# Performance work log

Measured on AMD Instinct MI355X. Metric: run time of the kernel, lower is better.

Reference implementation:

```python
import jax, jax.numpy as jnp
import numpy as np

DIM = 768
B, N = 8, 2048


def setup_inputs() -> dict:
    key = jax.random.key(0)
    k = jax.random.split(key, 8)
    s = 1.0 / np.sqrt(DIM)
    return {
        "x": jax.random.normal(k[0], (B, N, DIM), jnp.float32),
        "x2": jax.random.normal(k[1], (B, N, DIM), jnp.float32),
        "x3": jax.random.normal(k[2], (B, N, DIM), jnp.float32),
        "W1": jax.random.uniform(k[3], (DIM, DIM), jnp.float32, -s, s),
        "b1": jax.random.uniform(k[4], (DIM,), jnp.float32, -s, s),
        "W2": jax.random.uniform(k[5], (DIM, DIM), jnp.float32, -s, s),
        "b2": jax.random.uniform(k[6], (DIM,), jnp.float32, -s, s),
        "w": jnp.ones((1,), jnp.float32),
    }


def _cross_attention(x, x2, W, b):
    # key = softmax(x2.transpose(1,2), dim=1) -> softmax over feature axis, then [B, D, N]
    key = jnp.swapaxes(jax.nn.softmax(x2, axis=-1), 1, 2)  # [B, D, N]
    query = jax.nn.softmax(x2, axis=1)                      # [B, N, D], softmax over tokens
    context = jnp.einsum('bnd,bdm->bnm', x, key)            # [B, N, N]
    atten = jnp.einsum('bnm,bmd->bnd', context, query)      # [B, N, D]
    return atten @ W.T + b


def reference(x, x2, x3, W1, b1, W2, b2, w):
    a1 = _cross_attention(x, x2, W1, b1)
    a2 = _cross_attention(x, x3, W2, b2)
    f = jax.nn.sigmoid(w)  # scalar gate, broadcast
    atten = a1 * f + a2 * f
    return atten + x
```

## Files before the change

### kernel.cpp

```cpp
#include <hip/hip_runtime.h>

#define DIMD 768
#define NTOK 2048
#define NB   8

typedef __attribute__((ext_vector_type(8))) short bfrag8;
typedef __attribute__((ext_vector_type(4))) float accf4;

__device__ __forceinline__ unsigned short f2bf(float f) {
  unsigned u = __float_as_uint(f);
  return (unsigned short)((u + 0x7fffu + ((u >> 16) & 1u)) >> 16);
}

__device__ __forceinline__ void glds16(const void* g, void* l) {
  __builtin_amdgcn_global_load_lds(
      (const __attribute__((address_space(1))) void*)g,
      (__attribute__((address_space(3))) void*)l, 16, 0, 0);
}


__device__ __forceinline__ void packw_body(int blk, const float* __restrict__ W1,
                                           const float* __restrict__ W2,
                                           unsigned short* __restrict__ Wcat) {
  int gid = blk * 256 + threadIdx.x;
  int r = gid / 192, c4 = (gid % 192) * 4;
  float4 a = *(const float4*)(W1 + (size_t)r * DIMD + c4);
  float4 b = *(const float4*)(W2 + (size_t)r * DIMD + c4);
  union { unsigned short us[4]; uint2 u2; } ra, rb;
  ra.us[0] = f2bf(a.x); ra.us[1] = f2bf(a.y); ra.us[2] = f2bf(a.z); ra.us[3] = f2bf(a.w);
  rb.us[0] = f2bf(b.x); rb.us[1] = f2bf(b.y); rb.us[2] = f2bf(b.z); rb.us[3] = f2bf(b.w);
  *(uint2*)(Wcat + (size_t)r * 1536 + c4) = ra.u2;
  *(uint2*)(Wcat + (size_t)r * 1536 + 768 + c4) = rb.u2;
}

__device__ __forceinline__ void packx_body(int blk, const float* __restrict__ x,
                                           unsigned short* __restrict__ xb) {
  size_t gid = (size_t)blk * 256 + threadIdx.x;
  const float4* x4 = (const float4*)x;
  float4 v0 = x4[gid * 2], v1 = x4[gid * 2 + 1];
  union { unsigned short us[8]; uint4 u4; } r;
  r.us[0] = f2bf(v0.x); r.us[1] = f2bf(v0.y); r.us[2] = f2bf(v0.z); r.us[3] = f2bf(v0.w);
  r.us[4] = f2bf(v1.x); r.us[5] = f2bf(v1.y); r.us[6] = f2bf(v1.z); r.us[7] = f2bf(v1.w);
  ((uint4*)xb)[gid] = r.u4;
}

template <int TMD, int TND, int EPI>
__device__ __forceinline__ void gemm_body(
    unsigned short* As, unsigned short* Bs, int bid,
    const unsigned short* __restrict__ A, const unsigned short* __restrict__ B,
    void* __restrict__ Cout, int K, int lda, int ldb, int ldc, int ntx,
    long long sA, long long sB, long long sC,
    const float* __restrict__ wg, const float* __restrict__ b1v,
    const float* __restrict__ b2v, const float* __restrict__ xres) {
  constexpr int TM = 64 * TMD, TN = 64 * TND;
  constexpr int ASZ = TM * 64, BSZ = TN * 64;
  __shared__ float csi[64 * TND];
  const int t = threadIdx.x, w = t >> 6, lane = t & 63;
  const int bz = bid & 7;
  const int r = bid >> 3;
  const int by = r / ntx, bx = r - by * ntx;
  const int m0 = by * TM, n0 = bx * TN;
  const unsigned short* Ab = A + (size_t)bz * sA;
  const unsigned short* Bb = B + (size_t)bz * sB;
  const int srow = lane >> 3;
  const int scol = (lane & 7) * 8;

  auto stage = [&](int buf, int k0) {
    unsigned short* Ad = As + buf * ASZ;
    unsigned short* Bd = Bs + buf * BSZ;
#pragma unroll
    for (int l = 0; l < 2 * TND; ++l) {
      int chunk = l * 4 + w;
      int row = chunk * 8 + srow;
      glds16(Bb + (size_t)(n0 + row) * ldb + k0 + scol,
             (char*)Bd + chunk * 1024 + lane * 16);
    }
#pragma unroll
    for (int l = 0; l < 2 * TMD; ++l) {
      int chunk = l * 4 + w;
      int row = chunk * 8 + srow;
      glds16(Ab + (size_t)(m0 + row) * lda + k0 + scol,
             (char*)Ad + chunk * 1024 + lane * 16);
    }
  };

  stage(0, 0);

  if (EPI == 2) {
    for (int c = t; c < TN; c += 256) {
      const float* cp = b1v + (size_t)bz * 32 * DIMD + n0 + c;
      float s = 0.f;
#pragma unroll
      for (int p = 0; p < 32; ++p) s += cp[(size_t)p * DIMD];
      csi[c] = 1.0f / s;
    }
  }

  accf4 zero = {0.f, 0.f, 0.f, 0.f};
  accf4 acc[2 * TMD][2 * TND];
#pragma unroll
  for (int i = 0; i < 2 * TMD; ++i)
#pragma unroll
    for (int j = 0; j < 2 * TND; ++j) acc[i][j] = zero;

  const int wm = (w & 1) * (32 * TMD), wn = (w >> 1) * (32 * TND);
  const int lm = lane & 15, qd = lane >> 4;

  __syncthreads();

  const int nt = K / 64;
  int cur = 0;
#pragma unroll 2
  for (int tt = 0; tt < nt; ++tt) {
    if (tt + 1 < nt) stage(cur ^ 1, (tt + 1) * 64);
    const unsigned short* Ar = As + cur * ASZ;
    const unsigned short* Br = Bs + cur * BSZ;
#pragma unroll
    for (int kc = 0; kc < 2; ++kc) {
      bfrag8 av[2 * TMD], bv[2 * TND];
#pragma unroll
      for (int i = 0; i < 2 * TMD; ++i)
        av[i] = *(const bfrag8*)(Ar + (wm + i * 16 + lm) * 64 + kc * 32 + qd * 8);
#pragma unroll
      for (int j = 0; j < 2 * TND; ++j)
        bv[j] = *(const bfrag8*)(Br + (wn + j * 16 + lm) * 64 + kc * 32 + qd * 8);
      __builtin_amdgcn_s_setprio(1);
#pragma unroll
      for (int i = 0; i < 2 * TMD; ++i)
#pragma unroll
        for (int j = 0; j < 2 * TND; ++j)
          acc[i][j] = __builtin_amdgcn_mfma_f32_16x16x32_bf16(av[i], bv[j], acc[i][j], 0, 0, 0);
      __builtin_amdgcn_s_setprio(0);
    }
    if (tt + 1 < nt) {
      asm volatile("s_waitcnt vmcnt(0)\n\ts_barrier" ::: "memory");
    }
    cur ^= 1;
  }

  if (EPI == 0) {
    unsigned short* Cb = (unsigned short*)Cout + (size_t)bz * sC;
#pragma unroll
    for (int i = 0; i < 2 * TMD; ++i)
#pragma unroll
      for (int j = 0; j < 2 * TND; ++j) {
        int col = n0 + wn + j * 16 + lm;
#pragma unroll
        for (int rr = 0; rr < 4; ++rr) {
          int row = m0 + wm + i * 16 + qd * 4 + rr;
          Cb[(size_t)row * ldc + col] = f2bf(acc[i][j][rr]);
        }
      }
  } else if (EPI == 1) {
    float gate = 1.f / (1.f + __expf(-wg[0]));
    float* Co = (float*)Cout + (size_t)bz * sC;
    const float* Xr = xres + (size_t)bz * sC;
#pragma unroll
    for (int j = 0; j < 2 * TND; ++j) {
      int col = n0 + wn + j * 16 + lm;
      float gb = gate * (b1v[col] + b2v[col]);
#pragma unroll
      for (int i = 0; i < 2 * TMD; ++i)
#pragma unroll
        for (int rr = 0; rr < 4; ++rr) {
          int row = m0 + wm + i * 16 + qd * 4 + rr;
          size_t idx = (size_t)row * ldc + col;
          Co[idx] = gate * acc[i][j][rr] + gb + Xr[idx];
        }
    }
  } else {
    unsigned short* Cb = (unsigned short*)Cout + (size_t)bz * sC;
#pragma unroll
    for (int j = 0; j < 2 * TND; ++j) {
      int lc = wn + j * 16 + lm;
      int col = n0 + lc;
      float ci = csi[lc];
#pragma unroll
      for (int i = 0; i < 2 * TMD; ++i)
#pragma unroll
        for (int rr = 0; rr < 4; ++rr) {
          int row = m0 + wm + i * 16 + qd * 4 + rr;
          Cb[(size_t)row * ldc + col] = f2bf(acc[i][j][rr] * ci);
        }
    }
  }
}


__global__ __launch_bounds__(256) void prep_kernel(const float* __restrict__ W1,
                                                   const float* __restrict__ W2,
                                                   unsigned short* __restrict__ Wcat,
                                                   const float* __restrict__ x2,
                                                   const float* __restrict__ x3,
                                                   float* __restrict__ rs1,
                                                   float* __restrict__ rs2) {
  int blk = blockIdx.x;
  if (blk < 576) { packw_body(blk, W1, W2, Wcat); return; }
  int rblk = blk - 576;
  const float* src = (rblk < 4096) ? x2 : x3;
  float* dst = (rblk < 4096) ? rs1 : rs2;
  int q = rblk & 4095;
  int w = threadIdx.x >> 6, lane = threadIdx.x & 63;
  int row = q * 4 + w;
  const float* r = src + (size_t)row * DIMD;
  float s = 0.f;
#pragma unroll
  for (int j = 0; j < 12; ++j) s += __expf(r[lane + j * 64]);
#pragma unroll
  for (int off = 32; off; off >>= 1) s += __shfl_xor(s, off, 64);
  if (lane == 0) dst[row] = 1.0f / s;
}

__global__ __launch_bounds__(256) void sm_kq(
    const float* __restrict__ xA, const float* __restrict__ rsA,
    unsigned short* __restrict__ KtA, unsigned short* __restrict__ QtA,
    float* __restrict__ cspA,
    const float* __restrict__ xB, const float* __restrict__ rsB,
    unsigned short* __restrict__ KtB, unsigned short* __restrict__ QtB,
    float* __restrict__ cspB) {
  int z = blockIdx.z;
  const float* xin; const float* rsv; unsigned short* Kt; unsigned short* Qt;
  float* csp; int b;
  if (z < 8) { xin = xA; rsv = rsA; Kt = KtA; Qt = QtA; csp = cspA; b = z; }
  else       { xin = xB; rsv = rsB; Kt = KtB; Qt = QtB; csp = cspB; b = z - 8; }
  const int n0 = blockIdx.x * 64, dc = blockIdx.y;
  const int t = threadIdx.x;
  __shared__ float rowsi[64];
  __shared__ __align__(16) unsigned short etile[128 * 72];
  if (t < 64) rowsi[t] = rsv[(size_t)b * NTOK + n0 + t];
  const float* xbase = xin + ((size_t)b * NTOK + n0) * DIMD + dc * 128;
  const int tok = t >> 2, g0 = t & 3;
#pragma unroll
  for (int p = 0; p < 8; ++p) {
    int dg = g0 + p * 4;
    float4 v = *(const float4*)(xbase + (size_t)tok * DIMD + dg * 4);
    int dl = dg * 4;
    etile[(dl + 0) * 72 + tok] = f2bf(__expf(v.x));
    etile[(dl + 1) * 72 + tok] = f2bf(__expf(v.y));
    etile[(dl + 2) * 72 + tok] = f2bf(__expf(v.z));
    etile[(dl + 3) * 72 + tok] = f2bf(__expf(v.w));
  }
  __syncthreads();
#pragma unroll
  for (int q = 0; q < 4; ++q) {
    int dl = (t >> 3) + q * 32;
    int g = t & 7;
    uint4 e8 = *(const uint4*)(etile + dl * 72 + g * 8);
    float ef[8];
    ef[0] = __uint_as_float(e8.x << 16); ef[1] = __uint_as_float(e8.x & 0xffff0000u);
    ef[2] = __uint_as_float(e8.y << 16); ef[3] = __uint_as_float(e8.y & 0xffff0000u);
    ef[4] = __uint_as_float(e8.z << 16); ef[5] = __uint_as_float(e8.z & 0xffff0000u);
    ef[6] = __uint_as_float(e8.w << 16); ef[7] = __uint_as_float(e8.w & 0xffff0000u);
    float4 r0 = *(const float4*)&rowsi[g * 8];
    float4 r1 = *(const float4*)&rowsi[g * 8 + 4];
    union { unsigned short us[8]; uint4 u4; } ko;
    ko.us[0] = f2bf(ef[0] * r0.x); ko.us[1] = f2bf(ef[1] * r0.y);
    ko.us[2] = f2bf(ef[2] * r0.z); ko.us[3] = f2bf(ef[3] * r0.w);
    ko.us[4] = f2bf(ef[4] * r1.x); ko.us[5] = f2bf(ef[5] * r1.y);
    ko.us[6] = f2bf(ef[6] * r1.z); ko.us[7] = f2bf(ef[7] * r1.w);
    size_t orow = ((size_t)b * DIMD + dc * 128 + dl) * NTOK + n0 + g * 8;
    *(uint4*)(Kt + orow) = ko.u4;
    *(uint4*)(Qt + orow) = e8;
    float s = ((ef[0] + ef[1]) + (ef[2] + ef[3])) + ((ef[4] + ef[5]) + (ef[6] + ef[7]));
    s += __shfl_xor(s, 1, 64);
    s += __shfl_xor(s, 2, 64);
    s += __shfl_xor(s, 4, 64);
    if (g == 0) csp[((size_t)b * 32 + blockIdx.x) * DIMD + dc * 128 + dl] = s;
  }
}

template <int TMD, int TND, int EPI>
__global__ __launch_bounds__(256) void mfma_bt(
    const unsigned short* __restrict__ A, const unsigned short* __restrict__ B,
    void* __restrict__ Cout, int K, int lda, int ldb, int ldc, int ntx,
    long long sA, long long sB, long long sC,
    const float* __restrict__ wg, const float* __restrict__ b1v,
    const float* __restrict__ b2v, const float* __restrict__ xres) {
  __shared__ __align__(16) unsigned short As[2 * 64 * TMD * 64];
  __shared__ __align__(16) unsigned short Bs[2 * 64 * TND * 64];
  gemm_body<TMD, TND, EPI>(As, Bs, blockIdx.x, A, B, Cout, K, lda, ldb, ldc, ntx,
                           sA, sB, sC, wg, b1v, b2v, xres);
}

__global__ __launch_bounds__(256) void sgemm_s(
    const unsigned short* __restrict__ KtA, const unsigned short* __restrict__ QtA,
    const float* __restrict__ cspA,
    const unsigned short* __restrict__ KtB, const unsigned short* __restrict__ QtB,
    const float* __restrict__ cspB,
    unsigned short* __restrict__ Ca, unsigned short* __restrict__ Cb) {
  __shared__ __align__(16) unsigned short As[2 * 128 * 64];
  __shared__ __align__(16) unsigned short Bs[2 * 128 * 64];
  bool second = blockIdx.x >= 288;
  const unsigned short* A = second ? KtB : KtA;
  const unsigned short* B = second ? QtB : QtA;
  const float* csp = second ? cspB : cspA;
  unsigned short* C = second ? Cb : Ca;
  int blk = second ? (blockIdx.x - 288) : blockIdx.x;
  gemm_body<2, 2, 2>(As, Bs, blk, A, B, C, NTOK, NTOK, NTOK, 1536, 6,
                     768LL * NTOK, 768LL * NTOK, 768LL * 1536,
                     nullptr, csp, nullptr, nullptr);
}

__global__ __launch_bounds__(256) void s2_packx_kernel(
    const unsigned short* __restrict__ Wcat, const unsigned short* __restrict__ Scat,
    unsigned short* __restrict__ Bt, const float* __restrict__ x,
    unsigned short* __restrict__ xb) {
  __shared__ __align__(16) unsigned short As[2 * 128 * 64];
  __shared__ __align__(16) unsigned short Bs[2 * 128 * 64];
  int blk = blockIdx.x;
  if (blk < 288) {
    gemm_body<2, 2, 0>(As, Bs, blk, Wcat, Scat, Bt, 1536, 1536, 1536, 768, 6,
                       0LL, 768LL * 1536, 768LL * 768,
                       nullptr, nullptr, nullptr, nullptr);
  } else {
    packx_body(blk - 288, x, xb);
  }
}

extern "C" void kernel_launch(void* const* d_in, const int* in_sizes, int n_in,
                              void* d_out, int out_size, void* d_ws, size_t ws_size,
                              hipStream_t stream) {
  const float* x  = (const float*)d_in[0];
  const float* x2 = (const float*)d_in[1];
  const float* x3 = (const float*)d_in[2];
  const float* W1 = (const float*)d_in[3];
  const float* b1 = (const float*)d_in[4];
  const float* W2 = (const float*)d_in[5];
  const float* b2 = (const float*)d_in[6];
  const float* w  = (const float*)d_in[7];
  float* out = (float*)d_out;
  char* ws = (char*)d_ws;

  dim3 blk(256);
  const bool merged = ws_size >= 123600896ull;

  if (merged) {
    unsigned short* Kt1  = (unsigned short*)(ws + 0);
    unsigned short* Qt1  = (unsigned short*)(ws + 25165824);
    unsigned short* Kt2  = (unsigned short*)(ws + 50331648);
    unsigned short* Qt2  = (unsigned short*)(ws + 75497472);
    unsigned short* Scat = (unsigned short*)(ws + 100663296);
    unsigned short* Wcat = (unsigned short*)(ws + 119537664);
    float* csp1 = (float*)(ws + 121896960);
    float* csp2 = (float*)(ws + 122683392);
    float* rs1  = (float*)(ws + 123469824);
    float* rs2  = (float*)(ws + 123535360);
    unsigned short* Bt = (unsigned short*)(ws + 0);
    unsigned short* xb = (unsigned short*)(ws + 9437184);

    prep_kernel<<<8768, blk, 0, stream>>>(W1, W2, Wcat, x2, x3, rs1, rs2);
    sm_kq<<<dim3(32, 6, 16), blk, 0, stream>>>(x2, rs1, Kt1, Qt1, csp1,
                                               x3, rs2, Kt2, Qt2, csp2);
    sgemm_s<<<576, blk, 0, stream>>>(Kt1, Qt1, csp1, Kt2, Qt2, csp2, Scat, Scat + 768);
    s2_packx_kernel<<<6432, blk, 0, stream>>>(Wcat, Scat, Bt, x, xb);
    mfma_bt<2, 2, 1><<<768, blk, 0, stream>>>(xb, Bt, out, DIMD, DIMD, DIMD, DIMD, 6,
                                              (long long)NTOK * DIMD, 768LL * 768,
                                              (long long)NTOK * DIMD, w, b1, b2, x);
  } else {
    unsigned short* Kt   = (unsigned short*)(ws + 0);
    unsigned short* Qt   = (unsigned short*)(ws + 25165824);
    unsigned short* Scat = (unsigned short*)(ws + 50331648);
    unsigned short* Bt   = (unsigned short*)(ws + 69206016);
    float* csp1 = (float*)(ws + 69206016);
    float* csp2 = (float*)(ws + 69992448);
    float* rs1  = (float*)(ws + 70778880);
    float* rs2  = (float*)(ws + 70844416);
    unsigned short* xb   = (unsigned short*)(ws + 78643200);
    unsigned short* Wcat = (unsigned short*)(ws + 103809024);

    prep_kernel<<<8768, blk, 0, stream>>>(W1, W2, Wcat, x2, x3, rs1, rs2);
    sm_kq<<<dim3(32, 6, 8), blk, 0, stream>>>(x2, rs1, Kt, Qt, csp1,
                                              x2, rs1, Kt, Qt, csp1);
    sgemm_s<<<288, blk, 0, stream>>>(Kt, Qt, csp1, Kt, Qt, csp1, Scat, Scat);
    sm_kq<<<dim3(32, 6, 8), blk, 0, stream>>>(x3, rs2, Kt, Qt, csp2,
                                              x3, rs2, Kt, Qt, csp2);
    sgemm_s<<<288, blk, 0, stream>>>(Kt, Qt, csp2, Kt, Qt, csp2, Scat + 768, Scat + 768);
    s2_packx_kernel<<<6432, blk, 0, stream>>>(Wcat, Scat, Bt, x, xb);
    mfma_bt<2, 2, 1><<<768, blk, 0, stream>>>(xb, Bt, out, DIMD, DIMD, DIMD, DIMD, 6,
                                              (long long)NTOK * DIMD, 768LL * 768,
                                              (long long)NTOK * DIMD, w, b1, b2, x);
  }
}
```

Baseline: 356.2 us.

## Fuse row-softmax sums into K/Q build kernel and swizzle GEMM LDS tiles

Merges the separate row-sum prep pass and the softmax K/Q construction into one stage1 kernel. Each block now handles a full 768-wide token tile in LDS, so x2/x3 are read once instead of twice, and one launch is removed. Weight packing is folded into the same launch. Separately, the GEMM LDS staging and fragment reads are XOR-swizzled to reduce bank conflicts. The risks are the large LDS footprint per block (about 110KB), which limits occupancy, and fewer, longer blocks in the fused kernel.

```diff
diff --git a/kernel.cpp b/kernel.cpp
--- a/kernel.cpp
+++ b/kernel.cpp
@@ -63,7 +63,7 @@
   const unsigned short* Ab = A + (size_t)bz * sA;
   const unsigned short* Bb = B + (size_t)bz * sB;
   const int srow = lane >> 3;
-  const int scol = (lane & 7) * 8;
+  const int scol = (((lane & 7) ^ (lane >> 3)) * 8);
 
   auto stage = [&](int buf, int k0) {
     unsigned short* Ad = As + buf * ASZ;
@@ -105,6 +105,7 @@
 
   const int wm = (w & 1) * (32 * TMD), wn = (w >> 1) * (32 * TND);
   const int lm = lane & 15, qd = lane >> 4;
+  const int lsw = (lm & 7) << 3;
 
   __syncthreads();
 
@@ -118,12 +119,13 @@
 #pragma unroll
     for (int kc = 0; kc < 2; ++kc) {
       bfrag8 av[2 * TMD], bv[2 * TND];
+      const int kslot = (((kc << 2) | qd) << 3) ^ lsw;
 #pragma unroll
       for (int i = 0; i < 2 * TMD; ++i)
-        av[i] = *(const bfrag8*)(Ar + (wm + i * 16 + lm) * 64 + kc * 32 + qd * 8);
+        av[i] = *(const bfrag8*)(Ar + (wm + i * 16 + lm) * 64 + kslot);
 #pragma unroll
       for (int j = 0; j < 2 * TND; ++j)
-        bv[j] = *(const bfrag8*)(Br + (wn + j * 16 + lm) * 64 + kc * 32 + qd * 8);
+        bv[j] = *(const bfrag8*)(Br + (wn + j * 16 + lm) * 64 + kslot);
       __builtin_amdgcn_s_setprio(1);
 #pragma unroll
       for (int i = 0; i < 2 * TMD; ++i)
@@ -186,63 +188,51 @@
   }
 }
 
-
-__global__ __launch_bounds__(256) void prep_kernel(const float* __restrict__ W1,
-                                                   const float* __restrict__ W2,
-                                                   unsigned short* __restrict__ Wcat,
-                                                   const float* __restrict__ x2,
-                                                   const float* __restrict__ x3,
-                                                   float* __restrict__ rs1,
-                                                   float* __restrict__ rs2) {
+__global__ __launch_bounds__(256) void stage1_kernel(
+    const float* __restrict__ xA, unsigned short* __restrict__ KtA,
+    unsigned short* __restrict__ QtA, float* __restrict__ cspA,
+    const float* __restrict__ xB, unsigned short* __restrict__ KtB,
+    unsigned short* __restrict__ QtB, float* __restrict__ cspB,
+    int nsm,
+    const float* __restrict__ W1, const float* __restrict__ W2,
+    unsigned short* __restrict__ Wcat, int npw) {
   int blk = blockIdx.x;
-  if (blk < 576) { packw_body(blk, W1, W2, Wcat); return; }
-  int rblk = blk - 576;
-  const float* src = (rblk < 4096) ? x2 : x3;
-  float* dst = (rblk < 4096) ? rs1 : rs2;
-  int q = rblk & 4095;
-  int w = threadIdx.x >> 6, lane = threadIdx.x & 63;
-  int row = q * 4 + w;
-  const float* r = src + (size_t)row * DIMD;
+  if (blk >= nsm) {
+    if (blk < nsm + npw) packw_body(blk - nsm, W1, W2, Wcat);
+    return;
+  }
+  __shared__ float rowsi[64];
+  __shared__ __align__(16) unsigned short etile[768 * 72];
+  const int sel = blk >> 8;
+  const float* xin = sel ? xB : xA;
+  unsigned short* Kt = sel ? KtB : KtA;
+  unsigned short* Qt = sel ? QtB : QtA;
+  float* csp = sel ? cspB : cspA;
+  const int lb = blk & 255;
+  const int b = (lb >> 5) & 7, ntile = lb & 31, n0 = ntile * 64;
+  const int t = threadIdx.x;
+
+  const int tok = t >> 2, seg = t & 3;
+  const float* row = xin + ((size_t)b * NTOK + n0 + tok) * DIMD + seg * 192;
   float s = 0.f;
-#pragma unroll
-  for (int j = 0; j < 12; ++j) s += __expf(r[lane + j * 64]);
-#pragma unroll
-  for (int off = 32; off; off >>= 1) s += __shfl_xor(s, off, 64);
-  if (lane == 0) dst[row] = 1.0f / s;
-}
-
-__global__ __launch_bounds__(256) void sm_kq(
-    const float* __restrict__ xA, const float* __restrict__ rsA,
-    unsigned short* __restrict__ KtA, unsigned short* __restrict__ QtA,
-    float* __restrict__ cspA,
-    const float* __restrict__ xB, const float* __restrict__ rsB,
-    unsigned short* __restrict__ KtB, unsigned short* __restrict__ QtB,
-    float* __restrict__ cspB) {
-  int z = blockIdx.z;
-  const float* xin; const float* rsv; unsigned short* Kt; unsigned short* Qt;
-  float* csp; int b;
-  if (z < 8) { xin = xA; rsv = rsA; Kt = KtA; Qt = QtA; csp = cspA; b = z; }
-  else       { xin = xB; rsv = rsB; Kt = KtB; Qt = QtB; csp = cspB; b = z - 8; }
-  const int n0 = blockIdx.x * 64, dc = blockIdx.y;
-  const int t = threadIdx.x;
-  __shared__ float rowsi[64];
-  __shared__ __align__(16) unsigned short etile[128 * 72];
-  if (t < 64) rowsi[t] = rsv[(size_t)b * NTOK + n0 + t];
-  const float* xbase = xin + ((size_t)b * NTOK + n0) * DIMD + dc * 128;
-  const int tok = t >> 2, g0 = t & 3;
-#pragma unroll
-  for (int p = 0; p < 8; ++p) {
-    int dg = g0 + p * 4;
-    float4 v = *(const float4*)(xbase + (size_t)tok * DIMD + dg * 4);
-    int dl = dg * 4;
-    etile[(dl + 0) * 72 + tok] = f2bf(__expf(v.x));
-    etile[(dl + 1) * 72 + tok] = f2bf(__expf(v.y));
-    etile[(dl + 2) * 72 + tok] = f2bf(__expf(v.z));
-    etile[(dl + 3) * 72 + tok] = f2bf(__expf(v.w));
-  }
+#pragma unroll 12
+  for (int j = 0; j < 48; ++j) {
+    float4 v = *(const float4*)(row + j * 4);
+    float e0 = __expf(v.x), e1 = __expf(v.y), e2 = __expf(v.z), e3 = __expf(v.w);
+    s += (e0 + e1) + (e2 + e3);
+    int d = seg * 192 + j * 4;
+    etile[(d + 0) * 72 + tok] = f2bf(e0);
+    etile[(d + 1) * 72 + tok] = f2bf(e1);
+    etile[(d + 2) * 72 + tok] = f2bf(e2);
+    etile[(d + 3) * 72 + tok] = f2bf(e3);
+  }
+  s += __shfl_xor(s, 1, 64);
+  s += __shfl_xor(s, 2, 64);
+  if (seg == 0) rowsi[tok] = 1.0f / s;
   __syncthreads();
-#pragma unroll
-  for (int q = 0; q < 4; ++q) {
+
+#pragma unroll 4
+  for (int q = 0; q < 24; ++q) {
     int dl = (t >> 3) + q * 32;
     int g = t & 7;
     uint4 e8 = *(const uint4*)(etile + dl * 72 + g * 8);
@@ -258,14 +248,14 @@
     ko.us[2] = f2bf(ef[2] * r0.z); ko.us[3] = f2bf(ef[3] * r0.w);
     ko.us[4] = f2bf(ef[4] * r1.x); ko.us[5] = f2bf(ef[5] * r1.y);
     ko.us[6] = f2bf(ef[6] * r1.z); ko.us[7] = f2bf(ef[7] * r1.w);
-    size_t orow = ((size_t)b * DIMD + dc * 128 + dl) * NTOK + n0 + g * 8;
+    size_t orow = ((size_t)b * DIMD + dl) * NTOK + n0 + g * 8;
     *(uint4*)(Kt + orow) = ko.u4;
     *(uint4*)(Qt + orow) = e8;
-    float s = ((ef[0] + ef[1]) + (ef[2] + ef[3])) + ((ef[4] + ef[5]) + (ef[6] + ef[7]));
-    s += __shfl_xor(s, 1, 64);
-    s += __shfl_xor(s, 2, 64);
-    s += __shfl_xor(s, 4, 64);
-    if (g == 0) csp[((size_t)b * 32 + blockIdx.x) * DIMD + dc * 128 + dl] = s;
+    float cs = ((ef[0] + ef[1]) + (ef[2] + ef[3])) + ((ef[4] + ef[5]) + (ef[6] + ef[7]));
+    cs += __shfl_xor(cs, 1, 64);
+    cs += __shfl_xor(cs, 2, 64);
+    cs += __shfl_xor(cs, 4, 64);
+    if (g == 0) csp[((size_t)b * 32 + ntile) * DIMD + dl] = cs;
   }
 }
 
@@ -343,14 +333,12 @@
     unsigned short* Wcat = (unsigned short*)(ws + 119537664);
     float* csp1 = (float*)(ws + 121896960);
     float* csp2 = (float*)(ws + 122683392);
-    float* rs1  = (float*)(ws + 123469824);
-    float* rs2  = (float*)(ws + 123535360);
     unsigned short* Bt = (unsigned short*)(ws + 0);
     unsigned short* xb = (unsigned short*)(ws + 9437184);
 
-    prep_kernel<<<8768, blk, 0, stream>>>(W1, W2, Wcat, x2, x3, rs1, rs2);
-    sm_kq<<<dim3(32, 6, 16), blk, 0, stream>>>(x2, rs1, Kt1, Qt1, csp1,
-                                               x3, rs2, Kt2, Qt2, csp2);
+    stage1_kernel<<<1088, blk, 0, stream>>>(x2, Kt1, Qt1, csp1,
+                                            x3, Kt2, Qt2, csp2, 512,
+                                            W1, W2, Wcat, 576);
     sgemm_s<<<576, blk, 0, stream>>>(Kt1, Qt1, csp1, Kt2, Qt2, csp2, Scat, Scat + 768);
     s2_packx_kernel<<<6432, blk, 0, stream>>>(Wcat, Scat, Bt, x, xb);
     mfma_bt<2, 2, 1><<<768, blk, 0, stream>>>(xb, Bt, out, DIMD, DIMD, DIMD, DIMD, 6,
@@ -363,17 +351,16 @@
     unsigned short* Bt   = (unsigned short*)(ws + 69206016);
     float* csp1 = (float*)(ws + 69206016);
     float* csp2 = (float*)(ws + 69992448);
-    float* rs1  = (float*)(ws + 70778880);
-    float* rs2  = (float*)(ws + 70844416);
     unsigned short* xb   = (unsigned short*)(ws + 78643200);
     unsigned short* Wcat = (unsigned short*)(ws + 103809024);
 
-    prep_kernel<<<8768, blk, 0, stream>>>(W1, W2, Wcat, x2, x3, rs1, rs2);
-    sm_kq<<<dim3(32, 6, 8), blk, 0, stream>>>(x2, rs1, Kt, Qt, csp1,
-                                              x2, rs1, Kt, Qt, csp1);
+    stage1_kernel<<<832, blk, 0, stream>>>(x2, Kt, Qt, csp1,
+                                           x2, Kt, Qt, csp1, 256,
+                                           W1, W2, Wcat, 576);
     sgemm_s<<<288, blk, 0, stream>>>(Kt, Qt, csp1, Kt, Qt, csp1, Scat, Scat);
-    sm_kq<<<dim3(32, 6, 8), blk, 0, stream>>>(x3, rs2, Kt, Qt, csp2,
-                                              x3, rs2, Kt, Qt, csp2);
+    stage1_kernel<<<256, blk, 0, stream>>>(x3, Kt, Qt, csp2,
+                                           x3, Kt, Qt, csp2, 256,
+                                           W1, W2, Wcat, 0);
     sgemm_s<<<288, blk, 0, stream>>>(Kt, Qt, csp2, Kt, Qt, csp2, Scat + 768, Scat + 768);
     s2_packx_kernel<<<6432, blk, 0, stream>>>(Wcat, Scat, Bt, x, xb);
     mfma_bt<2, 2, 1><<<768, blk, 0, stream>>>(xb, Bt, out, DIMD, DIMD, DIMD, DIMD, 6,
```

Result: faster. 323.0 us (-9.3%).
